# Kernel optimization log

Measured on AMD Instinct MI355X. Metric: run time of the kernel, lower is better.

Reference implementation:

```python
import jax, jax.numpy as jnp
import numpy as np

B, S, D = 4, 4096, 1024
G, N, BLK, K = 8, 64, 8, 4
GD = D // G
NL = 24


def setup_inputs() -> dict:
    key = jax.random.key(0)
    ks = jax.random.split(key, 16)
    f32 = jnp.float32
    rn = lambda k, sh, s: jax.random.normal(k, sh, f32) * s
    inp = {}
    inp["x_r"] = jax.random.normal(ks[0], (B, S, D), f32)
    inp["x_i"] = jax.random.normal(ks[1], (B, S, D), f32)
    inp["norm_w"] = jnp.ones((D,), f32)
    inp["sg_theta"] = rn(ks[2], (D // BLK,), 0.1)
    inp["sg_Wg"] = rn(ks[3], (D, D), 1.0 / np.sqrt(D))
    inp["sg_bg"] = jnp.zeros((D,), f32)
    inp["conv_w"] = rn(ks[4], (2 * D, 2, K), 1.0 / np.sqrt(2 * K))
    inp["conv_b"] = jnp.zeros((2 * D,), f32)
    inp["log_A_mag"] = jax.random.uniform(ks[5], (G, N), f32) * 0.5 + 0.5
    inp["A_phase"] = rn(ks[6], (G, N), 0.1)
    inp["B_Wr"] = rn(ks[7], (N, GD), 1.0 / np.sqrt(GD))
    inp["B_Wi"] = rn(ks[8], (N, GD), 1.0 / np.sqrt(GD))
    inp["C_Wr"] = rn(ks[9], (GD, N), 1.0 / np.sqrt(N))
    inp["C_Wi"] = rn(ks[10], (GD, N), 1.0 / np.sqrt(N))
    inp["dt_W"] = rn(ks[11], (2, 2 * GD), 1.0 / np.sqrt(2 * GD))
    inp["dt_b"] = jnp.zeros((2,), f32)
    inp["out_Wr"] = rn(ks[12], (D, D), 1.0 / np.sqrt(D))
    inp["out_Wi"] = rn(ks[13], (D, D), 1.0 / np.sqrt(D))
    inp["act_thr"] = jnp.zeros((), f32)
    inp["ssm_scale"] = jnp.full((D,), 2.5, f32)
    inp["res_scale"] = jnp.asarray(1.0 / np.sqrt(2.0 * NL), f32)
    return inp


def reference(x_r, x_i, norm_w, sg_theta, sg_Wg, sg_bg, conv_w, conv_b,
              log_A_mag, A_phase, B_Wr, B_Wi, C_Wr, C_Wi, dt_W, dt_b,
              out_Wr, out_Wi, act_thr, ssm_scale, res_scale):
    b, s, d = x_r.shape
    g, n, gd = G, N, GD
    # --- ComplexRMSNorm: normalize by RMS of complex magnitude ---
    inv = jax.lax.rsqrt(jnp.mean(x_r * x_r + x_i * x_i, axis=-1, keepdims=True) + 1e-6)
    xr = x_r * inv * norm_w
    xi = x_i * inv * norm_w
    # --- SpinorGate: block-diagonal phase rotation with selective sigmoid gate ---
    theta = jnp.repeat(sg_theta, BLK)  # per-block angle broadcast to [D]
    mag = jnp.sqrt(xr * xr + xi * xi + 1e-8)
    gate = jax.nn.sigmoid(jnp.einsum('bsd,ed->bse', mag, sg_Wg) + sg_bg)
    ct, st = jnp.cos(theta), jnp.sin(theta)
    xr, xi = gate * (xr * ct - xi * st), gate * (xr * st + xi * ct)
    # --- grouped causal conv over interleaved real/imag channels ---
    x_il = jnp.stack([xr, xi], axis=-1).reshape(b, s, 2 * d).transpose(0, 2, 1)  # [B,2D,S]
    x_il = jnp.pad(x_il, ((0, 0), (0, 0), (K - 1, 0)))  # causal left pad
    co = jax.lax.conv_general_dilated(
        x_il, conv_w, (1,), 'VALID',
        dimension_numbers=('NCH', 'OIH', 'NCH'), feature_group_count=d)
    co = co + conv_b[None, :, None]
    co = co.transpose(0, 2, 1).reshape(b, s, d, 2)
    xr, xi = co[..., 0], co[..., 1]
    # --- magnitude-gated activation ---
    act = 1.0 - jnp.exp(-(xr * xr + xi * xi) * jnp.exp(act_thr))
    xr = xr * act
    xi = xi * act
    # --- MIMO groups ---
    xgr = xr.reshape(b, s, g, gd)
    xgi = xi.reshape(b, s, g, gd)
    # --- selective dt from concatenated real/imag features ---
    xcat = jnp.concatenate([xgr, xgi], axis=-1)  # [B,S,G,2*gd]
    dt = jnp.clip(jnp.exp(jnp.einsum('bsgd,ed->bsge', xcat, dt_W) + dt_b), 1e-4, 2.0)
    dt_mag, dt_ph = dt[..., 0:1], dt[..., 1:2]
    # --- discretized complex A (|A| < 1 guaranteed) ---
    a_mag = jnp.exp(dt_mag * (-jax.nn.softplus(log_A_mag)))  # [B,S,G,N]
    ang = dt_ph * A_phase
    ar = a_mag * jnp.cos(ang)
    ai = a_mag * jnp.sin(ang)
    # --- complex B projection ---
    bxr = (jnp.einsum('bsgd,nd->bsgn', xgr, B_Wr)
           - jnp.einsum('bsgd,nd->bsgn', xgi, B_Wi)) * dt_mag
    bxi = (jnp.einsum('bsgd,nd->bsgn', xgr, B_Wi)
           + jnp.einsum('bsgd,nd->bsgn', xgi, B_Wr)) * dt_mag
    # --- complex selective scan with renorm every 256 steps ---
    def step(carry, inp):
        hr, hi = carry
        a_r, a_i, b_r, b_i, t = inp
        nhr = a_r * hr - a_i * hi + b_r
        nhi = a_r * hi + a_i * hr + b_i
        hn = jnp.sqrt(nhr * nhr + nhi * nhi + 1e-8)
        sc = jnp.where((t + 1) % 256 == 0, jnp.minimum(hn, 100.0) / hn, 1.0)
        nhr = nhr * sc
        nhi = nhi * sc
        return (nhr, nhi), (nhr, nhi)

    h0 = jnp.zeros((b, g, n), x_r.dtype)
    mv = lambda a: jnp.moveaxis(a, 1, 0)  # [S,B,G,N]
    _, (Hr, Hi) = jax.lax.scan(step, (h0, h0),
                               (mv(ar), mv(ai), mv(bxr), mv(bxi), jnp.arange(s)))
    Hr = jnp.moveaxis(Hr, 0, 1)  # [B,S,G,N]
    Hi = jnp.moveaxis(Hi, 0, 1)
    # --- complex C projection ---
    yr = (jnp.einsum('bsgn,dn->bsgd', Hr, C_Wr)
          - jnp.einsum('bsgn,dn->bsgd', Hi, C_Wi)).reshape(b, s, d)
    yi = (jnp.einsum('bsgn,dn->bsgd', Hr, C_Wi)
          + jnp.einsum('bsgn,dn->bsgd', Hi, C_Wr)).reshape(b, s, d)
    # --- complex output projection, real per-channel scale, residual ---
    o_r = (jnp.einsum('bsd,ed->bse', yr, out_Wr)
           - jnp.einsum('bsd,ed->bse', yi, out_Wi)) * ssm_scale
    o_i = (jnp.einsum('bsd,ed->bse', yr, out_Wi)
           + jnp.einsum('bsd,ed->bse', yi, out_Wr)) * ssm_scale
    return jnp.stack([x_r + res_scale * o_r, x_i + res_scale * o_i], axis=-1)
```

## Files before the change

### kernel.cpp

```cpp
#include <hip/hip_runtime.h>
#include <hip/hip_bf16.h>
#include <hip/hip_fp8.h>
#include <math.h>

#define BB 4
#define SS 4096
#define DD 1024
#define GG 8
#define NN 64
#define GDIM 128
#define BS (BB*SS)
static const size_t BSD  = (size_t)BS * DD;
static const size_t BSGN = (size_t)BS * GG * NN;

typedef __attribute__((ext_vector_type(8))) short bf16x8;
typedef __attribute__((ext_vector_type(4))) float f32x4;
typedef __attribute__((ext_vector_type(4))) uint u32x4;
typedef unsigned char uchar;

__device__ inline ushort f2b(float x) {
    __hip_bfloat16 h = __float2bfloat16(x);
    return *reinterpret_cast<ushort*>(&h);
}
__device__ inline float b2f(ushort u) {
    union { uint q; float f; } x; x.q = ((uint)u) << 16; return x.f;
}
__device__ inline uchar f2fp8(float x) {
    __hip_fp8_e4m3 h(x);
    return *reinterpret_cast<uchar*>(&h);
}
__device__ __forceinline__ bf16x8 neg8(bf16x8 v) {
    union { bf16x8 b; u32x4 u; } x;
    x.b = v;
    x.u ^= 0x80008000u;
    return x.b;
}

#define GL16(gp, lp) __builtin_amdgcn_global_load_lds( \
    (const __attribute__((address_space(1))) void*)(gp), \
    (__attribute__((address_space(3))) void*)(lp), 16, 0, 0)

template<int KD, int LDA, int LDB>
__device__ __forceinline__ void mfma_core(
    const ushort* __restrict__ gA, const ushort* __restrict__ gB,
    ushort* lA, ushort* lB, int wave, int lane, f32x4 (&acc)[4][4])
{
    int r = lane & 15, h = lane >> 4;
    int wm = (wave & 1) * 64, wn = (wave >> 1) * 64;
    ushort* lA0 = lA + wave * 1024;
    ushort* lB0 = lB + wave * 1024;
    for (int k0 = 0; k0 < KD; k0 += 32) {
        __syncthreads();
        GL16(gA + k0,            lA0);
        GL16(gA + k0 + 16*LDA,   lA0 + 512);
        GL16(gB + k0,            lB0);
        GL16(gB + k0 + 16*LDB,   lB0 + 512);
        __syncthreads();
        bf16x8 af[4], bfv[4];
        #pragma unroll
        for (int i = 0; i < 4; i++) af[i]  = *(const bf16x8*)&lA[(wm + i*16 + r)*32 + h*8];
        #pragma unroll
        for (int j = 0; j < 4; j++) bfv[j] = *(const bf16x8*)&lB[(wn + j*16 + r)*32 + h*8];
        #pragma unroll
        for (int i = 0; i < 4; i++)
            #pragma unroll
            for (int j = 0; j < 4; j++)
                acc[i][j] = __builtin_amdgcn_mfma_f32_16x16x32_bf16(af[i], bfv[j], acc[i][j], 0, 0, 0);
    }
}

__global__ __launch_bounds__(256) void k_prep(
    const float* __restrict__ Wg, const float* __restrict__ BWr, const float* __restrict__ BWi,
    const float* __restrict__ CWr, const float* __restrict__ CWi,
    const float* __restrict__ Wor, const float* __restrict__ Woi,
    const float* __restrict__ logA, const float* __restrict__ theta,
    uchar* __restrict__ Wg8, ushort* __restrict__ BxT, ushort* __restrict__ A3,
    ushort* __restrict__ WoP, float* __restrict__ spl,
    float* __restrict__ ctab, float* __restrict__ stab)
{
    const int S1 = 1048576;
    const int S2 = S1 + 32768;
    const int S3 = S2 + 32768;
    const int S4 = S3 + 2097152;
    const int S5 = S4 + 512;
    const int S6 = S5 + 1024;
    const int S7 = S6 + 1024;
    for (int idx = blockIdx.x * 256 + threadIdx.x; idx < S7; idx += gridDim.x * 256) {
        if (idx < S1) {
            Wg8[idx] = f2fp8(Wg[idx] * 16.0f);
        } else if (idx < S2) {
            int j = idx - S1, n = j >> 8, kk = j & 255;
            float v;
            if (n < 64) v = (kk < 128) ? BWr[n*128 + kk] : -BWi[n*128 + (kk-128)];
            else { int n2 = n - 64; v = (kk < 128) ? BWi[n2*128 + kk] : BWr[n2*128 + (kk-128)]; }
            BxT[j] = f2b(v);
        } else if (idx < S3) {
            int j = idx - S2, m = j >> 8, kk = j & 255;
            float v;
            if (m < 64) v = (kk < 128) ? CWr[kk*64 + m] : -CWi[(kk-128)*64 + m];
            else { int n2 = m - 64; v = (kk < 128) ? CWi[kk*64 + n2] : CWr[(kk-128)*64 + n2]; }
            A3[j] = f2b(v);
        } else if (idx < S4) {
            int j = idx - S3, e = j >> 11, c = j & 2047;
            int g = c >> 8, kk = c & 255;
            float v = (kk < 128) ? Wor[(size_t)e*1024 + g*128 + kk]
                                 : Woi[(size_t)e*1024 + g*128 + (kk-128)];
            WoP[j] = f2b(v);
        } else if (idx < S5) {
            int j = idx - S4;
            spl[j] = log1pf(expf(logA[j]));
        } else if (idx < S6) {
            int j = idx - S5;
            ctab[j] = cosf(theta[j >> 3]);
        } else {
            int j = idx - S6;
            stab[j] = sinf(theta[j >> 3]);
        }
    }
}

__global__ __launch_bounds__(256) void k_pgemm(
    const ushort* __restrict__ A3, const ushort* __restrict__ WoP,
    ushort* __restrict__ Ppr, ushort* __restrict__ Ppi)
{
    __shared__ ushort lA[4096], lB[4096];
    int g = blockIdx.z;
    int bn = blockIdx.x * 128;
    int tid = threadIdx.x, wave = tid >> 6, lane = tid & 63;
    int row0 = wave*32 + (lane >> 2), col0 = (lane & 3) * 8;
    int r = lane & 15, h = lane >> 4;
    int wm = (wave & 1) * 64, wn = (wave >> 1) * 64;
    f32x4 acc[4][4] = {};
    mfma_core<256, 256, 2048>(A3 + (size_t)row0*256 + col0,
                              WoP + (size_t)(bn + row0)*2048 + g*256 + col0,
                              lA, lB, wave, lane, acc);
    #pragma unroll
    for (int i = 0; i < 4; i++) {
        int mb = wm + i*16 + h*4;
        #pragma unroll
        for (int j = 0; j < 4; j++) {
            int e = bn + wn + j*16 + r;
            #pragma unroll
            for (int t2 = 0; t2 < 4; t2++) {
                int m = mb + t2;
                float v = acc[i][j][t2];
                if (m < 64) {
                    Ppr[(size_t)e*512 + g*64 + m] = f2b(v);
                } else {
                    Ppi[(size_t)e*512 + g*64 + (m - 64)] = f2b(v);
                }
            }
        }
    }
}

__global__ __launch_bounds__(256) void k_norm(
    const float* __restrict__ xr_in, const float* __restrict__ xi_in,
    const float* __restrict__ norm_w,
    uchar* __restrict__ mag_o, float* __restrict__ inv_o)
{
    int row = blockIdx.x;
    int tid = threadIdx.x;
    size_t base = (size_t)row * DD;
    float4 vr = ((const float4*)(xr_in + base))[tid];
    float4 vi = ((const float4*)(xi_in + base))[tid];
    float ss = vr.x*vr.x + vr.y*vr.y + vr.z*vr.z + vr.w*vr.w
             + vi.x*vi.x + vi.y*vi.y + vi.z*vi.z + vi.w*vi.w;
    #pragma unroll
    for (int off = 32; off >= 1; off >>= 1) ss += __shfl_down(ss, off);
    __shared__ float ws4[4];
    if ((tid & 63) == 0) ws4[tid >> 6] = ss;
    __syncthreads();
    float tot = ws4[0] + ws4[1] + ws4[2] + ws4[3];
    float inv = rsqrtf(tot * (1.0f / DD) + 1e-6f);
    float4 w = ((const float4*)norm_w)[tid];
    vr.x *= inv * w.x; vr.y *= inv * w.y; vr.z *= inv * w.z; vr.w *= inv * w.w;
    vi.x *= inv * w.x; vi.y *= inv * w.y; vi.z *= inv * w.z; vi.w *= inv * w.w;
    uchar4 mb;
    mb.x = f2fp8(sqrtf(vr.x*vr.x + vi.x*vi.x + 1e-8f));
    mb.y = f2fp8(sqrtf(vr.y*vr.y + vi.y*vi.y + 1e-8f));
    mb.z = f2fp8(sqrtf(vr.z*vr.z + vi.z*vi.z + 1e-8f));
    mb.w = f2fp8(sqrtf(vr.w*vr.w + vi.w*vi.w + 1e-8f));
    ((uchar4*)(mag_o + base))[tid] = mb;
    if (tid == 0) inv_o[row] = inv;
}

__global__ __launch_bounds__(256) void k_gate_fp8(
    const uchar* __restrict__ A8, const uchar* __restrict__ B8,
    const float* __restrict__ bg, ushort* __restrict__ gate)
{
    __shared__ uchar lA[4096], lB[4096];
    int flat = blockIdx.y * 8 + blockIdx.x;
    int nid  = (flat & 7) * 128 + (flat >> 3);
    int bm = (nid >> 3) * 128, bn = (nid & 7) * 128;
    int tid = threadIdx.x, wave = tid >> 6, lane = tid & 63;
    int r = lane & 15, h = lane >> 4;
    int wm = (wave & 1) * 64, wn = (wave >> 1) * 64;
    int srow = wave*32 + (lane >> 1);
    int scol = (lane & 1) * 16;
    const uchar* gA = A8 + (size_t)(bm + srow)*1024 + scol;
    const uchar* gB = B8 + (size_t)(bn + srow)*1024 + scol;
    uchar* lA0 = lA + wave*1024;
    uchar* lB0 = lB + wave*1024;
    f32x4 acc[4][4] = {};
    for (int k0 = 0; k0 < 1024; k0 += 32) {
        __syncthreads();
        GL16(gA + k0, lA0);
        GL16(gB + k0, lB0);
        __syncthreads();
        long af[4], bfv[4];
        #pragma unroll
        for (int i = 0; i < 4; i++) af[i]  = *(const long*)&lA[(wm + i*16 + r)*32 + h*8];
        #pragma unroll
        for (int j = 0; j < 4; j++) bfv[j] = *(const long*)&lB[(wn + j*16 + r)*32 + h*8];
        #pragma unroll
        for (int i = 0; i < 4; i++)
            #pragma unroll
            for (int j = 0; j < 4; j++)
                acc[i][j] = __builtin_amdgcn_mfma_f32_16x16x32_fp8_fp8(af[i], bfv[j], acc[i][j], 0, 0, 0);
    }
    #pragma unroll
    for (int i = 0; i < 4; i++) {
        int mb = bm + wm + i*16 + h*4;
        #pragma unroll
        for (int j = 0; j < 4; j++) {
            int n = bn + wn + j*16 + r;
            float bias = bg[n];
            #pragma unroll
            for (int t2 = 0; t2 < 4; t2++) {
                float v = acc[i][j][t2] * 0.0625f + bias;
                gate[(size_t)(mb + t2)*DD + n] = f2b(1.0f / (1.0f + __expf(-v)));
            }
        }
    }
}

__global__ __launch_bounds__(256) void k_rotconv(
    const float* __restrict__ xr_raw, const float* __restrict__ xi_raw,
    const float* __restrict__ inv_, const float* __restrict__ norm_w,
    const ushort* __restrict__ gate,
    const float* __restrict__ ctab, const float* __restrict__ stab,
    const float* __restrict__ cw, const float* __restrict__ cb,
    const float* __restrict__ act_thr,
    const float* __restrict__ dtW, const float* __restrict__ dtb,
    ushort* __restrict__ xcat, float* __restrict__ dtm_o, float* __restrict__ dtp_o)
{
    const int CH = 16;
    int row0 = blockIdx.x * CH;
    int s0 = row0 & (SS - 1);
    int t = threadIdx.x, d0 = t * 4;
    int g = d0 >> 7, dd = d0 & 127;
    float4 w4  = *(const float4*)&norm_w[d0];
    float4 ct4 = *(const float4*)&ctab[d0];
    float4 st4 = *(const float4*)&stab[d0];
    float cwv[4][16];
    float cb0[4], cb1[4];
    #pragma unroll
    for (int j = 0; j < 4; j++) {
        #pragma unroll
        for (int q = 0; q < 4; q++)
            *(float4*)&cwv[j][q*4] = *(const float4*)&cw[(size_t)(2*(d0+j))*8 + q*4];
        cb0[j] = cb[2*(d0+j)];
        cb1[j] = cb[2*(d0+j) + 1];
    }
    float4 dtw0a = *(const float4*)&dtW[dd];
    float4 dtw0b = *(const float4*)&dtW[128 + dd];
    float4 dtw1a = *(const float4*)&dtW[256 + dd];
    float4 dtw1b = *(const float4*)&dtW[384 + dd];
    float ea  = __expf(act_thr[0]);
    float db0 = dtb[0], db1 = dtb[1];

    float p1r[4] = {}, p1i[4] = {}, p2r[4] = {}, p2i[4] = {}, p3r[4] = {}, p3i[4] = {};
    auto rotrow = [&](int rr, float (&orr)[4], float (&ori)[4]) {
        float4 a  = *(const float4*)&xr_raw[(size_t)rr*DD + d0];
        float4 bq = *(const float4*)&xi_raw[(size_t)rr*DD + d0];
        ushort4 gq = *(const ushort4*)&gate[(size_t)rr*DD + d0];
        float iv = inv_[rr];
        #pragma unroll
        for (int j = 0; j < 4; j++) {
            float ar = ((const float*)&a)[j]  * iv * ((const float*)&w4)[j];
            float ai = ((const float*)&bq)[j] * iv * ((const float*)&w4)[j];
            float c = ((const float*)&ct4)[j], s = ((const float*)&st4)[j];
            float gg = b2f(((const ushort*)&gq)[j]);
            orr[j] = gg * (ar*c - ai*s);
            ori[j] = gg * (ar*s + ai*c);
        }
    };
    if (s0 >= 1) rotrow(row0 - 1, p1r, p1i);
    if (s0 >= 2) rotrow(row0 - 2, p2r, p2i);
    if (s0 >= 3) rotrow(row0 - 3, p3r, p3i);

    for (int sl = 0; sl < CH; sl++) {
        int row = row0 + sl;
        float rr0[4], ri0[4];
        rotrow(row, rr0, ri0);
        float p0 = 0.f, p1 = 0.f;
        ushort4 ur, ui;
        #pragma unroll
        for (int j = 0; j < 4; j++) {
            float cr = cb0[j]
                + p3r[j]*cwv[j][0]  + p2r[j]*cwv[j][1]  + p1r[j]*cwv[j][2]  + rr0[j]*cwv[j][3]
                + p3i[j]*cwv[j][4]  + p2i[j]*cwv[j][5]  + p1i[j]*cwv[j][6]  + ri0[j]*cwv[j][7];
            float ci = cb1[j]
                + p3r[j]*cwv[j][8]  + p2r[j]*cwv[j][9]  + p1r[j]*cwv[j][10] + rr0[j]*cwv[j][11]
                + p3i[j]*cwv[j][12] + p2i[j]*cwv[j][13] + p1i[j]*cwv[j][14] + ri0[j]*cwv[j][15];
            float act = 1.0f - __expf(-(cr*cr + ci*ci) * ea);
            cr *= act; ci *= act;
            ((ushort*)&ur)[j] = f2b(cr);
            ((ushort*)&ui)[j] = f2b(ci);
            p0 += cr * ((const float*)&dtw0a)[j] + ci * ((const float*)&dtw0b)[j];
            p1 += cr * ((const float*)&dtw1a)[j] + ci * ((const float*)&dtw1b)[j];
        }
        *(ushort4*)&xcat[(size_t)row*2048 + g*256 + dd]       = ur;
        *(ushort4*)&xcat[(size_t)row*2048 + g*256 + 128 + dd] = ui;
        #pragma unroll
        for (int off = 16; off >= 1; off >>= 1) {
            p0 += __shfl_down(p0, off, 32);
            p1 += __shfl_down(p1, off, 32);
        }
        if ((t & 31) == 0) {
            dtm_o[(size_t)row*8 + g] = fminf(fmaxf(__expf(p0 + db0), 1e-4f), 2.0f);
            dtp_o[(size_t)row*8 + g] = fminf(fmaxf(__expf(p1 + db1), 1e-4f), 2.0f);
        }
        #pragma unroll
        for (int j = 0; j < 4; j++) {
            p3r[j] = p2r[j]; p3i[j] = p2i[j];
            p2r[j] = p1r[j]; p2i[j] = p1i[j];
            p1r[j] = rr0[j]; p1i[j] = ri0[j];
        }
    }
}

__global__ __launch_bounds__(256) void k_bx_mfma(
    const ushort* __restrict__ xcat, const ushort* __restrict__ BxT,
    const float* __restrict__ dtm_,
    float* __restrict__ br, float* __restrict__ bi)
{
    __shared__ ushort lA[4096], lB[4096];
    int g = blockIdx.z;
    int bm = blockIdx.y * 128;
    int tid = threadIdx.x, wave = tid >> 6, lane = tid & 63;
    int row0 = wave*32 + (lane >> 2), col0 = (lane & 3) * 8;
    int r = lane & 15, h = lane >> 4;
    int wm = (wave & 1) * 64, wn = (wave >> 1) * 64;
    f32x4 acc[4][4] = {};
    mfma_core<256, 2048, 256>(xcat + (size_t)(bm + row0)*2048 + g*256 + col0,
                              BxT + (size_t)row0*256 + col0,
                              lA, lB, wave, lane, acc);
    #pragma unroll
    for (int i = 0; i < 4; i++) {
        int mb = bm + wm + i*16 + h*4;
        #pragma unroll
        for (int j = 0; j < 4; j++) {
            int n = wn + j*16 + r;
            #pragma unroll
            for (int t2 = 0; t2 < 4; t2++) {
                int m = mb + t2;
                float v = acc[i][j][t2] * dtm_[(size_t)m*8 + g];
                if (n < 64) br[(size_t)m*512 + g*64 + n]      = v;
                else        bi[(size_t)m*512 + g*64 + n - 64] = v;
            }
        }
    }
}

__global__ __launch_bounds__(256) void k_scan1(
    const float* __restrict__ br, const float* __restrict__ bi,
    const float* __restrict__ dtm_, const float* __restrict__ dtp_,
    const float* __restrict__ spl_t, const float* __restrict__ aph,
    float* __restrict__ Sar, float* __restrict__ Sai,
    float* __restrict__ Sbr, float* __restrict__ Sbi)
{
    int blk = blockIdx.x;
    int half = blk & 1, c = (blk >> 1) & 63, b = blk >> 7;
    int t = half*256 + threadIdx.x;
    int g = t >> 6;
    float spl = spl_t[t], ap = aph[t];
    int row0 = b*SS + c*64;
    size_t idx = (size_t)row0 * 512 + t;
    const float* dtmp = dtm_ + (size_t)row0*8 + g;
    const float* dtpp = dtp_ + (size_t)row0*8 + g;
    float Ar = 1.f, Ai = 0.f, Br = 0.f, Bi = 0.f;
    for (int s0 = 0; s0 < 64; s0 += 4) {
        float vm[4], vp[4], wr[4], wi[4];
        #pragma unroll
        for (int u = 0; u < 4; u++) {
            vm[u] = dtmp[(s0+u)*8]; vp[u] = dtpp[(s0+u)*8];
            wr[u] = br[idx + (size_t)(s0+u)*512];
            wi[u] = bi[idx + (size_t)(s0+u)*512];
        }
        #pragma unroll
        for (int u = 0; u < 4; u++) {
            float am = __expf(-vm[u]*spl);
            float sa, ca; __sincosf(vp[u]*ap, &sa, &ca);
            float arv = am*ca, aiv = am*sa;
            float nBr = arv*Br - aiv*Bi + wr[u];
            float nBi = arv*Bi + aiv*Br + wi[u];
            float nAr = arv*Ar - aiv*Ai;
            float nAi = arv*Ai + aiv*Ar;
            Br = nBr; Bi = nBi; Ar = nAr; Ai = nAi;
        }
    }
    size_t o = ((size_t)(b*64 + c))*512 + t;
    Sar[o] = Ar; Sai[o] = Ai; Sbr[o] = Br; Sbi[o] = Bi;
}

__global__ __launch_bounds__(256) void k_scan2(
    const float* __restrict__ Sar, const float* __restrict__ Sai,
    const float* __restrict__ Sbr, const float* __restrict__ Sbi,
    float* __restrict__ hinr, float* __restrict__ hini)
{
    int blk = blockIdx.x;
    int half = blk & 1, b = blk >> 1;
    int t = half*256 + threadIdx.x;
    float hr = 0.f, hi = 0.f;
    for (int c = 0; c < 64; c++) {
        size_t o = ((size_t)(b*64 + c))*512 + t;
        hinr[o] = hr; hini[o] = hi;
        float nr = Sar[o]*hr - Sai[o]*hi + Sbr[o];
        float ni = Sar[o]*hi + Sai[o]*hr + Sbi[o];
        if ((c & 3) == 3) {
            float hn = sqrtf(nr*nr + ni*ni + 1e-8f);
            float sc = fminf(hn, 100.0f) / hn;
            nr *= sc; ni *= sc;
        }
        hr = nr; hi = ni;
    }
}

__global__ __launch_bounds__(256) void k_scan3(
    const float* __restrict__ br, const float* __restrict__ bi,
    const float* __restrict__ dtm_, const float* __restrict__ dtp_,
    const float* __restrict__ spl_t, const float* __restrict__ aph,
    const float* __restrict__ hinr, const float* __restrict__ hini,
    ushort* __restrict__ Hbf)
{
    int blk = blockIdx.x;
    int half = blk & 1, c = (blk >> 1) & 63, b = blk >> 7;
    int t = half*256 + threadIdx.x;
    int g = t >> 6;
    float spl = spl_t[t], ap = aph[t];
    int row0 = b*SS + c*64;
    size_t idx = (size_t)row0 * 512 + t;
    const float* dtmp = dtm_ + (size_t)row0*8 + g;
    const float* dtpp = dtp_ + (size_t)row0*8 + g;
    size_t o = ((size_t)(b*64 + c))*512 + t;
    float hr = hinr[o], hi = hini[o];
    bool rch = ((c & 3) == 3);
    for (int s0 = 0; s0 < 64; s0 += 4) {
        float vm[4], vp[4], wr[4], wi[4];
        #pragma unroll
        for (int u = 0; u < 4; u++) {
            vm[u] = dtmp[(s0+u)*8]; vp[u] = dtpp[(s0+u)*8];
            wr[u] = br[idx + (size_t)(s0+u)*512];
            wi[u] = bi[idx + (size_t)(s0+u)*512];
        }
        #pragma unroll
        for (int u = 0; u < 4; u++) {
            float am = __expf(-vm[u]*spl);
            float sa, ca; __sincosf(vp[u]*ap, &sa, &ca);
            float arv = am*ca, aiv = am*sa;
            float nr = arv*hr - aiv*hi + wr[u];
            float ni = arv*hi + aiv*hr + wi[u];
            if (rch && (s0 + u == 63)) {
                float hn = sqrtf(nr*nr + ni*ni + 1e-8f);
                float sc = fminf(hn, 100.0f) / hn;
                nr *= sc; ni *= sc;
            }
            size_t rb = (size_t)(row0 + s0 + u) * 1024;
            Hbf[rb + t]       = f2b(nr);
            Hbf[rb + 512 + t] = f2b(ni);
            hr = nr; hi = ni;
        }
    }
}

__global__ __launch_bounds__(256) void k_out_cplx(
    const ushort* __restrict__ A,
    const ushort* __restrict__ Ppr,
    const ushort* __restrict__ Ppi,
    const float* __restrict__ ssm,
    const float* __restrict__ xr0, const float* __restrict__ xi0,
    const float* __restrict__ res_scale, float* __restrict__ out)
{
    __shared__ ushort lHr[4096], lHi[4096], lPr[4096], lPi[4096];
    int flat = blockIdx.y * 8 + blockIdx.x;
    int nid  = (flat & 7) * 128 + (flat >> 3);
    int bm = (nid >> 3) * 128, be = (nid & 7) * 128;
    int tid = threadIdx.x, wave = tid >> 6, lane = tid & 63;
    int r = lane & 15, h = lane >> 4;
    int wm = (wave & 1) * 64, wn = (wave >> 1) * 64;
    int row0 = wave*32 + (lane >> 2), col0 = (lane & 3) * 8;
    const ushort* gHr = A + (size_t)(bm + row0)*1024 + col0;
    const ushort* gHi = gHr + 512;
    const ushort* gPr = Ppr + (size_t)(be + row0)*512 + col0;
    const ushort* gPi = Ppi + (size_t)(be + row0)*512 + col0;
    ushort* dHr = lHr + wave*1024;
    ushort* dHi = lHi + wave*1024;
    ushort* dPr = lPr + wave*1024;
    ushort* dPi = lPi + wave*1024;
    f32x4 accr[4][4] = {};
    f32x4 acci[4][4] = {};
    for (int k0 = 0; k0 < 512; k0 += 32) {
        __syncthreads();
        GL16(gHr + k0,           dHr);
        GL16(gHr + k0 + 16*1024, dHr + 512);
        GL16(gHi + k0,           dHi);
        GL16(gHi + k0 + 16*1024, dHi + 512);
        GL16(gPr + k0,           dPr);
        GL16(gPr + k0 + 16*512,  dPr + 512);
        GL16(gPi + k0,           dPi);
        GL16(gPi + k0 + 16*512,  dPi + 512);
        __syncthreads();
        bf16x8 hrf[4], hif[4], prf[4], pif[4], npif[4];
        #pragma unroll
        for (int i = 0; i < 4; i++) {
            int ro = (wm + i*16 + r)*32 + h*8;
            hrf[i] = *(const bf16x8*)&lHr[ro];
            hif[i] = *(const bf16x8*)&lHi[ro];
        }
        #pragma unroll
        for (int j = 0; j < 4; j++) {
            int ro = (wn + j*16 + r)*32 + h*8;
            prf[j] = *(const bf16x8*)&lPr[ro];
            pif[j] = *(const bf16x8*)&lPi[ro];
            npif[j] = neg8(pif[j]);
        }
        #pragma unroll
        for (int i = 0; i < 4; i++)
            #pragma unroll
            for (int j = 0; j < 4; j++) {
                accr[i][j] = __builtin_amdgcn_mfma_f32_16x16x32_bf16(hrf[i], prf[j], accr[i][j], 0, 0, 0);
                accr[i][j] = __builtin_amdgcn_mfma_f32_16x16x32_bf16(hif[i], npif[j], accr[i][j], 0, 0, 0);
                acci[i][j] = __builtin_amdgcn_mfma_f32_16x16x32_bf16(hrf[i], pif[j],  acci[i][j], 0, 0, 0);
                acci[i][j] = __builtin_amdgcn_mfma_f32_16x16x32_bf16(hif[i], prf[j],  acci[i][j], 0, 0, 0);
            }
    }
    float rs = res_scale[0];
    #pragma unroll
    for (int i = 0; i < 4; i++) {
        int mb = bm + wm + i*16 + h*4;
        #pragma unroll
        for (int j = 0; j < 4; j++) {
            int e = be + wn + j*16 + r;
            float sc = ssm[e] * rs;
            #pragma unroll
            for (int t2 = 0; t2 < 4; t2++) {
                size_t p = (size_t)(mb + t2)*DD + e;
                float2 v;
                v.x = xr0[p] + accr[i][j][t2]*sc;
                v.y = xi0[p] + acci[i][j][t2]*sc;
                *(float2*)&out[2*p] = v;
            }
        }
    }
}

extern "C" void kernel_launch(void* const* d_in, const int* in_sizes, int n_in,
                              void* d_out, int out_size, void* d_ws, size_t ws_size,
                              hipStream_t stream) {
    const float* x_r      = (const float*)d_in[0];
    const float* x_i      = (const float*)d_in[1];
    const float* norm_w   = (const float*)d_in[2];
    const float* sg_theta = (const float*)d_in[3];
    const float* sg_Wg    = (const float*)d_in[4];
    const float* sg_bg    = (const float*)d_in[5];
    const float* conv_w   = (const float*)d_in[6];
    const float* conv_b   = (const float*)d_in[7];
    const float* log_A    = (const float*)d_in[8];
    const float* A_phase  = (const float*)d_in[9];
    const float* B_Wr     = (const float*)d_in[10];
    const float* B_Wi     = (const float*)d_in[11];
    const float* C_Wr     = (const float*)d_in[12];
    const float* C_Wi     = (const float*)d_in[13];
    const float* dt_W     = (const float*)d_in[14];
    const float* dt_b     = (const float*)d_in[15];
    const float* out_Wr   = (const float*)d_in[16];
    const float* out_Wi   = (const float*)d_in[17];
    const float* act_thr  = (const float*)d_in[18];
    const float* ssm_s    = (const float*)d_in[19];
    const float* res_s    = (const float*)d_in[20];
    float* out = (float*)d_out;
    float* ws  = (float*)d_ws;

    ushort* gate  = (ushort*)ws;
    ushort* xcat  = (ushort*)(ws + BSD);
    uchar*  mag8  = (uchar*)(ws + 2*BSD);
    float*  br    = ws + 2*BSD + BSGN;
    float*  bi    = ws + 2*BSD + 2*BSGN;
    ushort* Hbf   = (ushort*)(ws + 2*BSD + 3*BSGN);
    float*  sm    = ws + 2*BSD + 4*BSGN;
    float*  dtm   = sm;
    float*  dtp   = sm + 131072;
    float*  Sar   = sm + 2*131072;
    float*  Sai   = sm + 3*131072;
    float*  Sbr   = sm + 4*131072;
    float*  Sbi   = sm + 5*131072;
    float*  hinr  = sm + 6*131072;
    float*  hini  = sm + 7*131072;
    float*  inv   = sm + 8*131072;
    float*  spl   = inv + 16384;
    float*  ctab  = spl + 512;
    float*  stab  = ctab + 1024;
    uchar*  Wg8   = (uchar*)(stab + 1024);
    ushort* BxT   = (ushort*)(stab + 1024 + 262144);
    ushort* A3    = BxT + 32768;
    ushort* WoP   = A3 + 32768;
    ushort* Ppr   = WoP + 2097152;
    ushort* Ppi   = Ppr + 524288;

    k_prep<<<2048, 256, 0, stream>>>(sg_Wg, B_Wr, B_Wi, C_Wr, C_Wi, out_Wr, out_Wi,
                                     log_A, sg_theta, Wg8, BxT, A3, WoP, spl, ctab, stab);
    k_pgemm<<<dim3(8, 1, 8), 256, 0, stream>>>(A3, WoP, Ppr, Ppi);
    k_norm<<<BS, 256, 0, stream>>>(x_r, x_i, norm_w, mag8, inv);
    k_gate_fp8<<<dim3(8, 128), 256, 0, stream>>>(mag8, Wg8, sg_bg, gate);
    k_rotconv<<<BS/16, 256, 0, stream>>>(x_r, x_i, inv, norm_w, gate, ctab, stab,
                                         conv_w, conv_b, act_thr, dt_W, dt_b,
                                         xcat, dtm, dtp);
    k_bx_mfma<<<dim3(1, 128, 8), 256, 0, stream>>>(xcat, BxT, dtm, br, bi);
    k_scan1<<<512, 256, 0, stream>>>(br, bi, dtm, dtp, spl, A_phase, Sar, Sai, Sbr, Sbi);
    k_scan2<<<8, 256, 0, stream>>>(Sar, Sai, Sbr, Sbi, hinr, hini);
    k_scan3<<<512, 256, 0, stream>>>(br, bi, dtm, dtp, spl, A_phase, hinr, hini, Hbf);
    k_out_cplx<<<dim3(8, 128), 256, 0, stream>>>(Hbf, Ppr, Ppi, ssm_s, x_r, x_i, res_s, out);
}
```

Baseline: 372.9 us.

## Load MFMA operands directly from global memory in complex output GEMM

```diff
diff --git a/kernel.cpp b/kernel.cpp
--- a/kernel.cpp
+++ b/kernel.cpp
@@ -483,54 +483,36 @@
     const float* __restrict__ xr0, const float* __restrict__ xi0,
     const float* __restrict__ res_scale, float* __restrict__ out)
 {
-    __shared__ ushort lHr[4096], lHi[4096], lPr[4096], lPi[4096];
     int flat = blockIdx.y * 8 + blockIdx.x;
-    int nid  = (flat & 7) * 128 + (flat >> 3);
-    int bm = (nid >> 3) * 128, be = (nid & 7) * 128;
+    int e_t = flat >> 7;
+    int m_t = flat & 127;
+    int bm = m_t * 128, be = e_t * 128;
     int tid = threadIdx.x, wave = tid >> 6, lane = tid & 63;
     int r = lane & 15, h = lane >> 4;
     int wm = (wave & 1) * 64, wn = (wave >> 1) * 64;
-    int row0 = wave*32 + (lane >> 2), col0 = (lane & 3) * 8;
-    const ushort* gHr = A + (size_t)(bm + row0)*1024 + col0;
-    const ushort* gHi = gHr + 512;
-    const ushort* gPr = Ppr + (size_t)(be + row0)*512 + col0;
-    const ushort* gPi = Ppi + (size_t)(be + row0)*512 + col0;
-    ushort* dHr = lHr + wave*1024;
-    ushort* dHi = lHi + wave*1024;
-    ushort* dPr = lPr + wave*1024;
-    ushort* dPi = lPi + wave*1024;
+    const ushort* aBase = A   + (size_t)(bm + wm + r)*1024 + h*8;
+    const ushort* pBr   = Ppr + (size_t)(be + wn + r)*512  + h*8;
+    const ushort* pBi   = Ppi + (size_t)(be + wn + r)*512  + h*8;
     f32x4 accr[4][4] = {};
     f32x4 acci[4][4] = {};
     for (int k0 = 0; k0 < 512; k0 += 32) {
-        __syncthreads();
-        GL16(gHr + k0,           dHr);
-        GL16(gHr + k0 + 16*1024, dHr + 512);
-        GL16(gHi + k0,           dHi);
-        GL16(gHi + k0 + 16*1024, dHi + 512);
-        GL16(gPr + k0,           dPr);
-        GL16(gPr + k0 + 16*512,  dPr + 512);
-        GL16(gPi + k0,           dPi);
-        GL16(gPi + k0 + 16*512,  dPi + 512);
-        __syncthreads();
         bf16x8 hrf[4], hif[4], prf[4], pif[4], npif[4];
         #pragma unroll
         for (int i = 0; i < 4; i++) {
-            int ro = (wm + i*16 + r)*32 + h*8;
-            hrf[i] = *(const bf16x8*)&lHr[ro];
-            hif[i] = *(const bf16x8*)&lHi[ro];
-        }
-        #pragma unroll
-        for (int j = 0; j < 4; j++) {
-            int ro = (wn + j*16 + r)*32 + h*8;
-            prf[j] = *(const bf16x8*)&lPr[ro];
-            pif[j] = *(const bf16x8*)&lPi[ro];
+            hrf[i] = *(const bf16x8*)(aBase + i*16384 + k0);
+            hif[i] = *(const bf16x8*)(aBase + i*16384 + 512 + k0);
+        }
+        #pragma unroll
+        for (int j = 0; j < 4; j++) {
+            prf[j] = *(const bf16x8*)(pBr + j*8192 + k0);
+            pif[j] = *(const bf16x8*)(pBi + j*8192 + k0);
             npif[j] = neg8(pif[j]);
         }
         #pragma unroll
         for (int i = 0; i < 4; i++)
             #pragma unroll
             for (int j = 0; j < 4; j++) {
-                accr[i][j] = __builtin_amdgcn_mfma_f32_16x16x32_bf16(hrf[i], prf[j], accr[i][j], 0, 0, 0);
+                accr[i][j] = __builtin_amdgcn_mfma_f32_16x16x32_bf16(hrf[i], prf[j],  accr[i][j], 0, 0, 0);
                 accr[i][j] = __builtin_amdgcn_mfma_f32_16x16x32_bf16(hif[i], npif[j], accr[i][j], 0, 0, 0);
                 acci[i][j] = __builtin_amdgcn_mfma_f32_16x16x32_bf16(hrf[i], pif[j],  acci[i][j], 0, 0, 0);
                 acci[i][j] = __builtin_amdgcn_mfma_f32_16x16x32_bf16(hif[i], prf[j],  acci[i][j], 0, 0, 0);
```

New measurement: 418.4 us. +12.2%, slower.
